# Kernel optimization log

Measured on AMD Instinct MI355X. Metric: run time of the kernel, lower is better.

## Reference

```python
import jax, jax.numpy as jnp
from jax import lax
import numpy as np

D = 20            # bits per code -> codebook size K = 2**D
K = 2 ** D
TEMP = 0.005
EPS = 1e-10
XSPLIT = 16
ALPHA = 1.0


def setup_inputs() -> dict:
    key = jax.random.key(0)
    x = jax.random.normal(key, (2, 128, D), dtype=jnp.float32)  # [B, N, d]
    return {"x": x}


def _book_t():
    # Deterministic {-1,+1} codebook, transposed: [D, K]
    idx = jnp.arange(K, dtype=jnp.int32)
    shifts = jnp.arange(D - 1, -1, -1, dtype=jnp.int32)
    bits = ((idx[:, None] >> shifts[None, :]) & 1).astype(jnp.float32)  # [K, D]
    return (bits * 2.0 - 1.0).T  # [D, K]


def _forward(x):
    B, N, _ = x.shape
    book_t = _book_t()                      # [D, K]
    num_splits = N // XSPLIT
    # [num_splits, B, XSPLIT, D] chunks, scanned to bound peak memory (mirrors torch chunking)
    xc = x.reshape(B, num_splits, XSPLIT, D).transpose(1, 0, 2, 3)

    def step(carry, x_chunk):
        entro_mean, mean_probs = carry
        l = (x_chunk @ book_t) / TEMP                    # [B, XSPLIT, K]
        probs = jax.nn.softmax(l, axis=-1)
        log_probs = jax.nn.log_softmax(l + EPS, axis=-1)  # eps shift, as in torch
        entropy = -jnp.sum(probs * log_probs, axis=-1)    # [B, XSPLIT]
        entro_mean = entro_mean + jnp.sum(entropy, axis=-1) / N
        # torch: probs.mean over all but last dim -> [K], broadcast-added to [B,K]
        mean_probs = mean_probs + probs.mean(axis=(0, 1))
        return (entro_mean, mean_probs), None

    init = (jnp.zeros((B,), x.dtype), jnp.zeros((K,), x.dtype))
    (entro_mean, mean_probs), _ = lax.scan(jax.checkpoint(step), init, xc)

    mean_probs = mean_probs / num_splits
    # torch mean_probs rows are identical across batch, so mean over batch == single row value
    mean_entro = -jnp.sum(mean_probs * jnp.log(mean_probs + EPS))
    entro_mean_s = entro_mean.mean()
    entro_loss = ALPHA * entro_mean_s - ALPHA * mean_entro

    q_hard = jnp.where(x > 0, 1.0, -1.0).astype(x.dtype)
    q = x + lax.stop_gradient(q_hard - x)                 # straight-through estimator
    commit_loss = jnp.mean((x - lax.stop_gradient(q)) ** 2)
    return q, entro_mean_s, mean_entro, entro_loss, commit_loss


def reference(x):
    return _forward(x)
```

## Files before the change

kernel.cpp:

```cpp
#include <hip/hip_runtime.h>
#include <math.h>


#define RS 264
#define POISON 0xAAAAAAAAu

typedef float f32x4 __attribute__((ext_vector_type(4)));
typedef short bf16x8 __attribute__((ext_vector_type(8)));

__device__ inline unsigned short pk_bf16(float a) {
  unsigned ua = __float_as_uint(a);
  ua += 0x7FFFu + ((ua >> 16) & 1u);
  return (unsigned short)(ua >> 16);
}

__global__ __launch_bounds__(512) void lfq_one(
    const float* __restrict__ x, float* __restrict__ out,
    double* __restrict__ entPart, double* __restrict__ comPart,
    double* __restrict__ mePart, unsigned* __restrict__ counter) {
  const int blk = blockIdx.x;
  const int tid = threadIdx.x;

  __shared__ unsigned short sP[128 * RS];
  __shared__ double red[512];
  __shared__ float hb[20], cb[20];
  __shared__ int lastBlk;

  if (tid < 20) {
    float xv = x[blk * 20 + tid];
    float z = 400.f * xv, az = fabsf(z);
    float e = __expf(-az), s = e / (1.f + e);
    hb[tid] = log1pf(e) + az * s;
    float qv = (xv > 0.f) ? 1.f : -1.f;
    out[blk * 20 + tid] = qv;
    float dx = xv - qv;
    cb[tid] = dx * dx;
  }

  {
    const int side = tid >> 8;
    const int t = tid & 255;
    const int jo = side * 10;
    const int hi4 = side ? (blk >> 4) : (blk & 15);

    float p[10];
    const float2* xp = (const float2*)(x + t * 20 + jo);
#pragma unroll
    for (int k = 0; k < 5; ++k) {
      float2 v = xp[k];
      float zz0 = 400.f * v.x, zz1 = 400.f * v.y;
      float a0 = fabsf(zz0), a1 = fabsf(zz1);
      float e0 = __expf(-a0), e1 = __expf(-a1);
      float s0 = e0 / (1.f + e0), s1 = e1 / (1.f + e1);
      p[2 * k]     = (zz0 >= 0.f) ? (1.f - s0) : s0;
      p[2 * k + 1] = (zz1 >= 0.f) ? (1.f - s1) : s1;
    }
    float c = 1.f;
#pragma unroll
    for (int j = 0; j < 4; ++j)
      c *= ((hi4 >> (3 - j)) & 1) ? p[j] : (1.f - p[j]);
    float cvh[8], vl[8];
#pragma unroll
    for (int g = 0; g < 8; ++g) {
      cvh[g] = c * ((g & 4) ? p[4] : 1.f - p[4])
                 * ((g & 2) ? p[5] : 1.f - p[5])
                 * ((g & 1) ? p[6] : 1.f - p[6]);
      vl[g]  =     ((g & 4) ? p[7] : 1.f - p[7])
                 * ((g & 2) ? p[8] : 1.f - p[8])
                 * ((g & 1) ? p[9] : 1.f - p[9]);
    }
    unsigned short* panel = sP + side * 64 * RS;
#pragma unroll
    for (int r = 0; r < 64; ++r)
      panel[r * RS + t] = pk_bf16(cvh[r >> 3] * vl[r & 7]);
  }
  __syncthreads();

  if (tid == 0) {
    float hs = 0.f, cs = 0.f;
#pragma unroll
    for (int j = 0; j < 20; ++j) { hs += hb[j]; cs += cb[j]; }
    entPart[blk] = (double)hs;
    comPart[blk] = (double)cs;
  }

  const int lane = tid & 63, w = tid >> 6;
  const int m16 = lane & 15, q = lane >> 4;
  const unsigned short* ap = sP + ((w & 3) * 16 + m16) * RS + q * 8;
  const unsigned short* bp = sP + (64 + (w >> 2) * 32 + m16) * RS + q * 8;
  f32x4 acc0 = {0.f, 0.f, 0.f, 0.f}, acc1 = {0.f, 0.f, 0.f, 0.f};
#pragma unroll
  for (int ks = 0; ks < 8; ++ks) {
    bf16x8 af = *(const bf16x8*)(ap + ks * 32);
    bf16x8 b0 = *(const bf16x8*)(bp + ks * 32);
    bf16x8 b1 = *(const bf16x8*)(bp + 16 * RS + ks * 32);
    acc0 = __builtin_amdgcn_mfma_f32_16x16x32_bf16(af, b0, acc0, 0, 0, 0);
    acc1 = __builtin_amdgcn_mfma_f32_16x16x32_bf16(af, b1, acc1, 0, 0, 0);
  }

  float ts = 0.f;
#pragma unroll
  for (int i = 0; i < 4; ++i) {
    float m0 = acc0[i] * (1.f / 256.f);
    ts -= m0 * __logf(m0 + 1e-10f);
    float m1 = acc1[i] * (1.f / 256.f);
    ts -= m1 * __logf(m1 + 1e-10f);
  }
  red[tid] = (double)ts;
  __syncthreads();
  for (int s = 256; s > 0; s >>= 1) {
    if (tid < s) red[tid] += red[tid + s];
    __syncthreads();
  }
  if (tid == 0) {
    mePart[blk] = red[0];
    __threadfence();
    unsigned old = atomicAdd(counter, 1u);
    lastBlk = ((old - POISON) == 255u) ? 1 : 0;
  }
  __syncthreads();

  if (lastBlk) {
    __threadfence();
    __shared__ double r1[256], r2[256], r3[256];
    if (tid < 256) {
      r1[tid] = entPart[tid];
      r2[tid] = comPart[tid];
      r3[tid] = mePart[tid];
    }
    __syncthreads();
    for (int s = 128; s > 0; s >>= 1) {
      if (tid < s) {
        r1[tid] += r1[tid + s];
        r2[tid] += r2[tid + s];
        r3[tid] += r3[tid + s];
      }
      __syncthreads();
    }
    if (tid == 0) {
      double em = r1[0] / 256.0;
      double cm = r2[0] / 5120.0;
      double me = r3[0];
      out[5120] = (float)em;
      out[5121] = (float)me;
      out[5122] = (float)(em - me);
      out[5123] = (float)cm;
    }
  }
}

extern "C" void kernel_launch(void* const* d_in, const int* in_sizes, int n_in,
                              void* d_out, int out_size, void* d_ws, size_t ws_size,
                              hipStream_t stream) {
  const float* x = (const float*)d_in[0];
  float* out = (float*)d_out;
  char* ws = (char*)d_ws;
  double* entPart = (double*)(ws);
  double* comPart = (double*)(ws + 2048);
  double* mePart  = (double*)(ws + 4096);
  unsigned* counter = (unsigned*)(ws + 6144);

  lfq_one<<<256, 512, 0, stream>>>(x, out, entPart, comPart, mePart, counter);
}
```

Before: 63.09 us.

## Use wave shuffles for reductions and a two-level completion counter

Replaces the shared-memory tree reductions, which needed many barriers, with wavefront shuffle reductions plus a small per-wave partial array. Partials are now stored as float instead of double. The single global atomic counter, hit by all 256 blocks, becomes 16 strided counters plus a second-level counter, to spread atomic contention. Using float accumulation slightly changes numerical precision, and correctness depends on the workspace counters being poisoned to the expected value.

```diff
diff --git a/kernel.cpp b/kernel.cpp
--- a/kernel.cpp
+++ b/kernel.cpp
@@ -16,25 +16,36 @@
 
 __global__ __launch_bounds__(512) void lfq_one(
     const float* __restrict__ x, float* __restrict__ out,
-    double* __restrict__ entPart, double* __restrict__ comPart,
-    double* __restrict__ mePart, unsigned* __restrict__ counter) {
+    float* __restrict__ entP, float* __restrict__ comP,
+    float* __restrict__ meP, unsigned* __restrict__ cnt1,
+    unsigned* __restrict__ cnt2) {
   const int blk = blockIdx.x;
   const int tid = threadIdx.x;
+  const int lane = tid & 63, w = tid >> 6;
 
   __shared__ unsigned short sP[128 * RS];
-  __shared__ double red[512];
-  __shared__ float hb[20], cb[20];
+  __shared__ float wpart[8];
+  __shared__ float fe[8], fc[8], fm[8];
   __shared__ int lastBlk;
 
-  if (tid < 20) {
-    float xv = x[blk * 20 + tid];
-    float z = 400.f * xv, az = fabsf(z);
-    float e = __expf(-az), s = e / (1.f + e);
-    hb[tid] = log1pf(e) + az * s;
-    float qv = (xv > 0.f) ? 1.f : -1.f;
-    out[blk * 20 + tid] = qv;
-    float dx = xv - qv;
-    cb[tid] = dx * dx;
+  if (tid < 64) {
+    float h = 0.f, cterm = 0.f;
+    if (tid < 20) {
+      float xv = x[blk * 20 + tid];
+      float z = 400.f * xv, az = fabsf(z);
+      float e = __expf(-az), s = e / (1.f + e);
+      h = log1pf(e) + az * s;
+      float qv = (xv > 0.f) ? 1.f : -1.f;
+      out[blk * 20 + tid] = qv;
+      float dx = xv - qv;
+      cterm = dx * dx;
+    }
+#pragma unroll
+    for (int off = 32; off > 0; off >>= 1) {
+      h += __shfl_down(h, off, 64);
+      cterm += __shfl_down(cterm, off, 64);
+    }
+    if (tid == 0) { entP[blk] = h; comP[blk] = cterm; }
   }
 
   {
@@ -76,15 +87,6 @@
   }
   __syncthreads();
 
-  if (tid == 0) {
-    float hs = 0.f, cs = 0.f;
-#pragma unroll
-    for (int j = 0; j < 20; ++j) { hs += hb[j]; cs += cb[j]; }
-    entPart[blk] = (double)hs;
-    comPart[blk] = (double)cs;
-  }
-
-  const int lane = tid & 63, w = tid >> 6;
   const int m16 = lane & 15, q = lane >> 4;
   const unsigned short* ap = sP + ((w & 3) * 16 + m16) * RS + q * 8;
   const unsigned short* bp = sP + (64 + (w >> 2) * 32 + m16) * RS + q * 8;
@@ -106,41 +108,47 @@
     float m1 = acc1[i] * (1.f / 256.f);
     ts -= m1 * __logf(m1 + 1e-10f);
   }
-  red[tid] = (double)ts;
+#pragma unroll
+  for (int off = 32; off > 0; off >>= 1) ts += __shfl_down(ts, off, 64);
+  if (lane == 0) wpart[w] = ts;
   __syncthreads();
-  for (int s = 256; s > 0; s >>= 1) {
-    if (tid < s) red[tid] += red[tid + s];
-    __syncthreads();
-  }
+
   if (tid == 0) {
-    mePart[blk] = red[0];
+    float s = 0.f;
+#pragma unroll
+    for (int i = 0; i < 8; ++i) s += wpart[i];
+    meP[blk] = s;
     __threadfence();
-    unsigned old = atomicAdd(counter, 1u);
-    lastBlk = ((old - POISON) == 255u) ? 1 : 0;
+    unsigned o1 = atomicAdd(&cnt1[(blk & 15) * 32], 1u);
+    int last = 0;
+    if (o1 - POISON == 15u) {
+      __threadfence();
+      unsigned o2 = atomicAdd(cnt2, 1u);
+      last = (o2 - POISON == 15u);
+    }
+    lastBlk = last;
   }
   __syncthreads();
 
   if (lastBlk) {
     __threadfence();
-    __shared__ double r1[256], r2[256], r3[256];
-    if (tid < 256) {
-      r1[tid] = entPart[tid];
-      r2[tid] = comPart[tid];
-      r3[tid] = mePart[tid];
+    float e = 0.f, cs = 0.f, m = 0.f;
+    if (tid < 256) { e = entP[tid]; cs = comP[tid]; m = meP[tid]; }
+#pragma unroll
+    for (int off = 32; off > 0; off >>= 1) {
+      e  += __shfl_down(e, off, 64);
+      cs += __shfl_down(cs, off, 64);
+      m  += __shfl_down(m, off, 64);
     }
+    if (lane == 0) { fe[w] = e; fc[w] = cs; fm[w] = m; }
     __syncthreads();
-    for (int s = 128; s > 0; s >>= 1) {
-      if (tid < s) {
-        r1[tid] += r1[tid + s];
-        r2[tid] += r2[tid + s];
-        r3[tid] += r3[tid + s];
-      }
-      __syncthreads();
-    }
     if (tid == 0) {
-      double em = r1[0] / 256.0;
-      double cm = r2[0] / 5120.0;
-      double me = r3[0];
+      float E = 0.f, C = 0.f, M = 0.f;
+#pragma unroll
+      for (int i = 0; i < 8; ++i) { E += fe[i]; C += fc[i]; M += fm[i]; }
+      double em = (double)E / 256.0;
+      double cm = (double)C / 5120.0;
+      double me = (double)M;
       out[5120] = (float)em;
       out[5121] = (float)me;
       out[5122] = (float)(em - me);
@@ -155,10 +163,11 @@
   const float* x = (const float*)d_in[0];
   float* out = (float*)d_out;
   char* ws = (char*)d_ws;
-  double* entPart = (double*)(ws);
-  double* comPart = (double*)(ws + 2048);
-  double* mePart  = (double*)(ws + 4096);
-  unsigned* counter = (unsigned*)(ws + 6144);
+  float* entP = (float*)(ws);
+  float* comP = (float*)(ws + 1024);
+  float* meP  = (float*)(ws + 2048);
+  unsigned* cnt1 = (unsigned*)(ws + 4096);
+  unsigned* cnt2 = (unsigned*)(ws + 4096 + 16 * 128);
 
-  lfq_one<<<256, 512, 0, stream>>>(x, out, entPart, comPart, mePart, counter);
+  lfq_one<<<256, 512, 0, stream>>>(x, out, entP, comP, meP, cnt1, cnt2);
 }
```

Result: no change. 62.93 us (-0.3%).
